# Kernel tuning notes

Hardware: AMD Instinct MI355X
Metric: run time of the kernel (lower is better)

## Reference

```python
import jax, jax.numpy as jnp
import numpy as np

B, R, N, E, D, H = 4, 10, 64, 64, 300, 512  # batch, rounds, nodes, neighbours(=nodes), numberbatch_dim, lstm_hidden
SLOPE = 0.2  # LeakyReLU negative slope from config['slope']


def _xavier_uniform(key, shape, gain=1.414):
    fan_in, fan_out = shape[0], shape[1]
    lim = gain * np.sqrt(6.0 / (fan_in + fan_out))
    return jax.random.uniform(key, shape, jnp.float32, -lim, lim)


def setup_inputs() -> dict:
    key = jax.random.key(0)
    k0, k1, k2, k3, k4 = jax.random.split(key, 5)
    return {
        "adj_list": jax.random.normal(k0, (B, R, N, E, D), jnp.float32),
        "original_nodes": jax.random.normal(k1, (B, R, N, D), jnp.float32),
        "ques_embed": jax.random.normal(k2, (B, R, H), jnp.float32),
        "W": _xavier_uniform(k3, (D + H, H)),
        "a": _xavier_uniform(k4, (2 * H, 1)),
    }


def reference(adj_list, original_nodes, ques_embed, W, a):
    d_in = original_nodes.shape[-1]
    h = W.shape[-1]
    # Split W so that concat([x, q]) @ W == x @ Wn + q @ Wq (avoids the explicit
    # repeat + concat in the original torch code; same math).
    Wn, Wq = W[:d_in], W[d_in:]
    q_proj = jnp.einsum('brq,qh->brh', ques_embed, Wq)              # (B,R,H)
    w_original = jnp.einsum('brnd,dh->brnh', original_nodes, Wn) + q_proj[:, :, None, :]      # (B,R,N,H)
    Wh = jnp.einsum('brned,dh->brneh', adj_list, Wn) + q_proj[:, :, None, None, :]            # (B,R,N,E,H)
    a1, a2 = a[:h, 0], a[h:, 0]
    # e[b,r,n,e] = leakyrelu( (w_original @ a1)[b,r,n] + (Wh @ a2)[b,r,n,e] )
    scores = jnp.einsum('brnh,h->brn', w_original, a1)[..., None] + jnp.einsum('brneh,h->brne', Wh, a2)
    scores = jnp.where(scores > 0, scores, SLOPE * scores)
    # Faithful to original: softmax over dim=1 (the rounds axis). Dropout omitted (eval mode).
    attn = jax.nn.softmax(scores, axis=1)                            # (B,R,N,E)
    # h_prime[b,r,i,h] = sum_j attn[b,r,i,j] * w_original[b,r,j,h]  (requires E == N)
    h_prime = jnp.einsum('brij,brjh->brih', attn, w_original)
    return jax.nn.elu(h_prime)  # concat=True branch
```

## Files before the change

### kernel.cpp

```cpp
#include <hip/hip_runtime.h>
#include <math.h>

namespace {
constexpr int B = 4, R = 10, N = 64, E = 64, D = 300, H = 512;
constexpr int BR = B * R;
constexpr int NE = N * E;
constexpr int S = BR * NE;
constexpr float SLOPE = 0.2f;
constexpr int WO_BLOCKS = BR * 8;
constexpr int S2_BLOCKS = S / 64;

constexpr int OFF_V1  = 0;
constexpr int OFF_V2  = OFF_V1 + 300;
constexpr int OFF_U1  = OFF_V2 + 300;
constexpr int OFF_U2  = OFF_U1 + H;
constexpr int OFF_QP  = OFF_U2 + H;
constexpr int OFF_QA1 = OFF_QP + BR * H;
constexpr int OFF_QA2 = OFF_QA1 + BR;
constexpr int OFF_S1  = OFF_QA2 + BR;
constexpr int OFF_RAW = OFF_S1 + BR * N;
constexpr int OFF_WO  = OFF_RAW + S;
}

__device__ inline float waveReduce(float v) {
#pragma unroll
  for (int o = 32; o > 0; o >>= 1) v += __shfl_xor(v, o, 64);
  return v;
}

__device__ inline float dot4(float4 a, float4 b) {
  return a.x * b.x + a.y * b.y + a.z * b.z + a.w * b.w;
}

__global__ __launch_bounds__(64) void k_vecs(const float* __restrict__ W,
                                             const float* __restrict__ a,
                                             float* __restrict__ ws) {
  int row = blockIdx.x;
  int lane = threadIdx.x;
  const float4* rf  = reinterpret_cast<const float4*>(W + (size_t)row * H);
  const float4* a1f = reinterpret_cast<const float4*>(a);
  const float4* a2f = reinterpret_cast<const float4*>(a + H);
  float4 x0 = rf[lane], x1 = rf[64 + lane];
  float4 p0 = a1f[lane], p1 = a1f[64 + lane];
  float4 q0 = a2f[lane], q1 = a2f[64 + lane];
  float s1 = dot4(x0, p0) + dot4(x1, p1);
  float s2 = dot4(x0, q0) + dot4(x1, q1);
  s1 = waveReduce(s1);
  s2 = waveReduce(s2);
  if (lane == 0) {
    if (row < D) { ws[OFF_V1 + row] = s1; ws[OFF_V2 + row] = s2; }
    else         { ws[OFF_U1 + (row - D)] = s1; ws[OFF_U2 + (row - D)] = s2; }
  }
}

__global__ __launch_bounds__(512) void k_qproj_s1(const float* __restrict__ ques,
                                                  const float* __restrict__ W,
                                                  const float* __restrict__ orig,
                                                  float* __restrict__ ws) {
  int br = blockIdx.x, h = threadIdx.x;
  __shared__ float qs[H];
  __shared__ float red[16];
  __shared__ float qa1s;
  qs[h] = ques[(size_t)br * H + h];
  __syncthreads();
  float ac0 = 0.f, ac1 = 0.f, ac2 = 0.f, ac3 = 0.f;
#pragma unroll 4
  for (int q = 0; q < H; q += 4) {
    ac0 = fmaf(qs[q + 0], W[(size_t)(D + q + 0) * H + h], ac0);
    ac1 = fmaf(qs[q + 1], W[(size_t)(D + q + 1) * H + h], ac1);
    ac2 = fmaf(qs[q + 2], W[(size_t)(D + q + 2) * H + h], ac2);
    ac3 = fmaf(qs[q + 3], W[(size_t)(D + q + 3) * H + h], ac3);
  }
  float acc = (ac0 + ac1) + (ac2 + ac3);
  ws[OFF_QP + br * H + h] = acc;
  float p1 = qs[h] * ws[OFF_U1 + h];
  float p2 = qs[h] * ws[OFF_U2 + h];
  p1 = waveReduce(p1);
  p2 = waveReduce(p2);
  int lane = h & 63, wave = h >> 6;
  if (lane == 0) { red[wave] = p1; red[8 + wave] = p2; }
  __syncthreads();
  if (h == 0) {
    float t1 = 0.f, t2 = 0.f;
#pragma unroll
    for (int i = 0; i < 8; ++i) { t1 += red[i]; t2 += red[8 + i]; }
    ws[OFF_QA1 + br] = t1;
    ws[OFF_QA2 + br] = t2;
    qa1s = t1;
  }
  __syncthreads();
  float qa1 = qa1s;
  const float4* vf = reinterpret_cast<const float4*>(ws + OFF_V1);
  float4 va = vf[lane];
  float4 vb = (lane < 11) ? vf[64 + lane] : make_float4(0.f, 0.f, 0.f, 0.f);
  for (int n2 = wave * 8; n2 < wave * 8 + 8; n2 += 2) {
    const float4* rf0 = reinterpret_cast<const float4*>(orig + ((size_t)br * N + n2) * D);
    const float4* rf1 = reinterpret_cast<const float4*>(orig + ((size_t)br * N + n2 + 1) * D);
    float a0 = dot4(rf0[lane], va);
    float a1 = dot4(rf1[lane], va);
    if (lane < 11) {
      a0 += dot4(rf0[64 + lane], vb);
      a1 += dot4(rf1[64 + lane], vb);
    }
#pragma unroll
    for (int o = 32; o > 0; o >>= 1) {
      a0 += __shfl_xor(a0, o, 64);
      a1 += __shfl_xor(a1, o, 64);
    }
    if (lane == 0) {
      ws[OFF_S1 + br * N + n2]     = a0 + qa1;
      ws[OFF_S1 + br * N + n2 + 1] = a1 + qa1;
    }
  }
}

__global__ __launch_bounds__(256) void k_s2_wo(const float* __restrict__ adj,
                                               const float* __restrict__ orig,
                                               const float* __restrict__ W,
                                               float* __restrict__ ws) {
  __shared__ __align__(16) float smem[64 * 30 + 30 * 64];
  int t = threadIdx.x;
  if (blockIdx.x < WO_BLOCKS) {
    int bi = blockIdx.x;
    int br = bi >> 3, h0 = (bi & 7) * 64;
    float* sA = smem;
    float* sB = smem + 1920;
    const float4* sBf = reinterpret_cast<const float4*>(sB);
    int tn = t >> 4, th = t & 15;
    float acc[4][4] = {};
    for (int k0 = 0; k0 < D; k0 += 30) {
      __syncthreads();
      for (int idx = t; idx < 64 * 30; idx += 256) {
        int n = idx / 30, kk = idx % 30;
        sA[idx] = orig[((size_t)br * N + n) * D + k0 + kk];
      }
      for (int idx = t; idx < 30 * 64; idx += 256) {
        int kk = idx >> 6, hh = idx & 63;
        sB[idx] = W[(size_t)(k0 + kk) * H + h0 + hh];
      }
      __syncthreads();
#pragma unroll 5
      for (int kk = 0; kk < 30; ++kk) {
        float av[4];
#pragma unroll
        for (int i = 0; i < 4; ++i) av[i] = sA[(tn * 4 + i) * 30 + kk];
        float4 bv = sBf[kk * 16 + th];
#pragma unroll
        for (int i = 0; i < 4; ++i) {
          acc[i][0] = fmaf(av[i], bv.x, acc[i][0]);
          acc[i][1] = fmaf(av[i], bv.y, acc[i][1]);
          acc[i][2] = fmaf(av[i], bv.z, acc[i][2]);
          acc[i][3] = fmaf(av[i], bv.w, acc[i][3]);
        }
      }
    }
#pragma unroll
    for (int i = 0; i < 4; ++i) {
      int n = tn * 4 + i;
#pragma unroll
      for (int j = 0; j < 4; ++j) {
        int h = h0 + th * 4 + j;
        ws[OFF_WO + ((size_t)br * N + n) * H + h] = acc[i][j] + ws[OFF_QP + br * H + h];
      }
    }
    return;
  }
  for (int i = t; i < 300; i += 256) smem[i] = ws[OFF_V2 + i];
  __syncthreads();
  const float4* v4 = reinterpret_cast<const float4*>(smem);
  int grp = t & 3;
  int row = (blockIdx.x - WO_BLOCKS) * 64 + (t >> 2);
  const float4* ap = reinterpret_cast<const float4*>(adj) + (size_t)row * 75;
  float ac0 = 0.f, ac1 = 0.f;
#pragma unroll
  for (int j = 0; j < 19; ++j) {
    int idx = grp + 4 * j;
    if (j < 18 || grp < 3) {
      float4 x = ap[idx];
      float4 v = v4[idx];
      if (j & 1) ac1 = fmaf(x.x, v.x, fmaf(x.y, v.y, fmaf(x.z, v.z, fmaf(x.w, v.w, ac1))));
      else       ac0 = fmaf(x.x, v.x, fmaf(x.y, v.y, fmaf(x.z, v.z, fmaf(x.w, v.w, ac0))));
    }
  }
  float acc = ac0 + ac1;
  acc += __shfl_xor(acc, 1, 64);
  acc += __shfl_xor(acc, 2, 64);
  if (grp == 0) ws[OFF_RAW + row] = acc;
}

__global__ __launch_bounds__(256) void k_hprime(const float* __restrict__ ws,
                                                float* __restrict__ out) {
  int br = blockIdx.x;
  int b = br / R, r = br % R;
  int t = threadIdx.x;
  __shared__ __align__(16) float sAtt[64 * 64];
  const float* raw = ws + OFF_RAW;
  for (int ne = t; ne < NE; ne += 256) {
    int n = ne >> 6;
    float v[R];
    float m = -1e30f;
#pragma unroll
    for (int rr = 0; rr < R; ++rr) {
      int brr = b * R + rr;
      float sc = raw[(size_t)brr * NE + ne] + ws[OFF_QA2 + brr] + ws[OFF_S1 + brr * N + n];
      sc = sc > 0.f ? sc : SLOPE * sc;
      v[rr] = sc;
      m = fmaxf(m, sc);
    }
    float s = 0.f;
#pragma unroll
    for (int rr = 0; rr < R; ++rr) { v[rr] = __expf(v[rr] - m); s += v[rr]; }
    sAtt[ne] = v[r] / s;
  }
  __syncthreads();
  int h = blockIdx.y * 64 + (t & 63);
  int ig = t >> 6;
  float acc[16] = {};
  const float* wo = ws + OFF_WO + (size_t)br * N * H;
  const float4* sAttf = reinterpret_cast<const float4*>(sAtt);
#pragma unroll 2
  for (int j4 = 0; j4 < 16; ++j4) {
    float w0 = wo[(size_t)(4 * j4 + 0) * H + h];
    float w1 = wo[(size_t)(4 * j4 + 1) * H + h];
    float w2 = wo[(size_t)(4 * j4 + 2) * H + h];
    float w3 = wo[(size_t)(4 * j4 + 3) * H + h];
#pragma unroll
    for (int ii = 0; ii < 16; ++ii) {
      float4 a4 = sAttf[(ig * 16 + ii) * 16 + j4];
      acc[ii] = fmaf(a4.x, w0, fmaf(a4.y, w1, fmaf(a4.z, w2, fmaf(a4.w, w3, acc[ii]))));
    }
  }
#pragma unroll
  for (int ii = 0; ii < 16; ++ii) {
    int i = ig * 16 + ii;
    float x = acc[ii];
    out[((size_t)br * N + i) * H + h] = x > 0.f ? x : expm1f(x);
  }
}

extern "C" void kernel_launch(void* const* d_in, const int* in_sizes, int n_in,
                              void* d_out, int out_size, void* d_ws, size_t ws_size,
                              hipStream_t stream) {
  const float* adj  = (const float*)d_in[0];
  const float* orig = (const float*)d_in[1];
  const float* ques = (const float*)d_in[2];
  const float* W    = (const float*)d_in[3];
  const float* a    = (const float*)d_in[4];
  float* out = (float*)d_out;
  float* ws  = (float*)d_ws;

  k_vecs<<<dim3(D + H), dim3(64), 0, stream>>>(W, a, ws);
  k_qproj_s1<<<dim3(BR), dim3(512), 0, stream>>>(ques, W, orig, ws);
  k_s2_wo<<<dim3(WO_BLOCKS + S2_BLOCKS), dim3(256), 0, stream>>>(adj, orig, W, ws);
  k_hprime<<<dim3(BR, 8), dim3(256), 0, stream>>>(ws, out);
}
```

Baseline: 122.1 us.

## Split round-axis softmax into its own kernel and widen adj dot-product rows

Moves the leaky-ReLU plus rounds-axis softmax out of k_hprime into a separate k_softmax kernel. It runs once per (b, n, e) and writes normalized attention to workspace, so the 8 h-blocks per br no longer recompute all 10 rounds of softmax redundantly. The adj score kernel now uses 8 lanes per row with all loads issued up front, which raises memory-level parallelism and doubles the block count. The cost is one extra kernel launch and an extra workspace round-trip for the attention matrix.

```diff
diff --git a/kernel.cpp b/kernel.cpp
--- a/kernel.cpp
+++ b/kernel.cpp
@@ -8,7 +8,8 @@
 constexpr int S = BR * NE;
 constexpr float SLOPE = 0.2f;
 constexpr int WO_BLOCKS = BR * 8;
-constexpr int S2_BLOCKS = S / 64;
+constexpr int S2_ROWS = 32;
+constexpr int S2_BLOCKS = S / S2_ROWS;
 
 constexpr int OFF_V1  = 0;
 constexpr int OFF_V2  = OFF_V1 + 300;
@@ -19,7 +20,8 @@
 constexpr int OFF_QA2 = OFF_QA1 + BR;
 constexpr int OFF_S1  = OFF_QA2 + BR;
 constexpr int OFF_RAW = OFF_S1 + BR * N;
-constexpr int OFF_WO  = OFF_RAW + S;
+constexpr int OFF_SC  = OFF_RAW + S;
+constexpr int OFF_WO  = OFF_SC + S;
 }
 
 __device__ inline float waveReduce(float v) {
@@ -114,10 +116,10 @@
   }
 }
 
-__global__ __launch_bounds__(256) void k_s2_wo(const float* __restrict__ adj,
-                                               const float* __restrict__ orig,
-                                               const float* __restrict__ W,
-                                               float* __restrict__ ws) {
+__global__ __launch_bounds__(256) void k_s2wo(const float* __restrict__ adj,
+                                              const float* __restrict__ orig,
+                                              const float* __restrict__ W,
+                                              float* __restrict__ ws) {
   __shared__ __align__(16) float smem[64 * 30 + 30 * 64];
   int t = threadIdx.x;
   if (blockIdx.x < WO_BLOCKS) {
@@ -168,53 +170,61 @@
   for (int i = t; i < 300; i += 256) smem[i] = ws[OFF_V2 + i];
   __syncthreads();
   const float4* v4 = reinterpret_cast<const float4*>(smem);
-  int grp = t & 3;
-  int row = (blockIdx.x - WO_BLOCKS) * 64 + (t >> 2);
+  int row = (blockIdx.x - WO_BLOCKS) * S2_ROWS + (t >> 3);
+  int g = t & 7;
   const float4* ap = reinterpret_cast<const float4*>(adj) + (size_t)row * 75;
-  float ac0 = 0.f, ac1 = 0.f;
-#pragma unroll
-  for (int j = 0; j < 19; ++j) {
-    int idx = grp + 4 * j;
-    if (j < 18 || grp < 3) {
-      float4 x = ap[idx];
-      float4 v = v4[idx];
-      if (j & 1) ac1 = fmaf(x.x, v.x, fmaf(x.y, v.y, fmaf(x.z, v.z, fmaf(x.w, v.w, ac1))));
-      else       ac0 = fmaf(x.x, v.x, fmaf(x.y, v.y, fmaf(x.z, v.z, fmaf(x.w, v.w, ac0))));
-    }
-  }
-  float acc = ac0 + ac1;
+  float4 L0 = ap[g +  0], L1 = ap[g +  8], L2 = ap[g + 16];
+  float4 L3 = ap[g + 24], L4 = ap[g + 32], L5 = ap[g + 40];
+  float4 L6 = ap[g + 48], L7 = ap[g + 56], L8 = ap[g + 64];
+  float4 L9 = make_float4(0.f, 0.f, 0.f, 0.f);
+  float4 V9 = L9;
+  if (g < 3) { L9 = ap[g + 72]; V9 = v4[g + 72]; }
+  float4 V0 = v4[g +  0], V1 = v4[g +  8], V2 = v4[g + 16];
+  float4 V3 = v4[g + 24], V4 = v4[g + 32], V5 = v4[g + 40];
+  float4 V6 = v4[g + 48], V7 = v4[g + 56], V8 = v4[g + 64];
+  float a0 = dot4(L0, V0) + dot4(L2, V2) + dot4(L4, V4) + dot4(L6, V6) + dot4(L8, V8);
+  float a1 = dot4(L1, V1) + dot4(L3, V3) + dot4(L5, V5) + dot4(L7, V7) + dot4(L9, V9);
+  float acc = a0 + a1;
   acc += __shfl_xor(acc, 1, 64);
   acc += __shfl_xor(acc, 2, 64);
-  if (grp == 0) ws[OFF_RAW + row] = acc;
+  acc += __shfl_xor(acc, 4, 64);
+  if (g == 0) ws[OFF_RAW + row] = acc;
+}
+
+__global__ __launch_bounds__(256) void k_softmax(float* __restrict__ ws) {
+  int t = blockIdx.x * 256 + threadIdx.x;
+  int b = t >> 12;
+  int ne = t & 4095;
+  int n = ne >> 6;
+  const float* raw = ws + OFF_RAW;
+  float v[R];
+  float m = -1e30f;
+#pragma unroll
+  for (int r = 0; r < R; ++r) {
+    int br = b * R + r;
+    float sc = raw[(size_t)br * NE + ne] + ws[OFF_QA2 + br] + ws[OFF_S1 + br * N + n];
+    sc = sc > 0.f ? sc : SLOPE * sc;
+    v[r] = sc;
+    m = fmaxf(m, sc);
+  }
+  float s = 0.f;
+#pragma unroll
+  for (int r = 0; r < R; ++r) { v[r] = __expf(v[r] - m); s += v[r]; }
+  float inv = 1.f / s;
+#pragma unroll
+  for (int r = 0; r < R; ++r)
+    ws[OFF_SC + (size_t)(b * R + r) * NE + ne] = v[r] * inv;
 }
 
 __global__ __launch_bounds__(256) void k_hprime(const float* __restrict__ ws,
                                                 float* __restrict__ out) {
   int br = blockIdx.x;
-  int b = br / R, r = br % R;
-  int t = threadIdx.x;
+  int h = blockIdx.y * 64 + (threadIdx.x & 63);
+  int ig = threadIdx.x >> 6;
   __shared__ __align__(16) float sAtt[64 * 64];
-  const float* raw = ws + OFF_RAW;
-  for (int ne = t; ne < NE; ne += 256) {
-    int n = ne >> 6;
-    float v[R];
-    float m = -1e30f;
-#pragma unroll
-    for (int rr = 0; rr < R; ++rr) {
-      int brr = b * R + rr;
-      float sc = raw[(size_t)brr * NE + ne] + ws[OFF_QA2 + brr] + ws[OFF_S1 + brr * N + n];
-      sc = sc > 0.f ? sc : SLOPE * sc;
-      v[rr] = sc;
-      m = fmaxf(m, sc);
-    }
-    float s = 0.f;
-#pragma unroll
-    for (int rr = 0; rr < R; ++rr) { v[rr] = __expf(v[rr] - m); s += v[rr]; }
-    sAtt[ne] = v[r] / s;
-  }
-  __syncthreads();
-  int h = blockIdx.y * 64 + (t & 63);
-  int ig = t >> 6;
+  const float* att = ws + OFF_SC + (size_t)br * NE;
+  for (int idx = threadIdx.x; idx < 4096; idx += 256) sAtt[idx] = att[idx];
+  __syncthreads();
   float acc[16] = {};
   const float* wo = ws + OFF_WO + (size_t)br * N * H;
   const float4* sAttf = reinterpret_cast<const float4*>(sAtt);
@@ -251,6 +261,7 @@
 
   k_vecs<<<dim3(D + H), dim3(64), 0, stream>>>(W, a, ws);
   k_qproj_s1<<<dim3(BR), dim3(512), 0, stream>>>(ques, W, orig, ws);
-  k_s2_wo<<<dim3(WO_BLOCKS + S2_BLOCKS), dim3(256), 0, stream>>>(adj, orig, W, ws);
+  k_s2wo<<<dim3(WO_BLOCKS + S2_BLOCKS), dim3(256), 0, stream>>>(adj, orig, W, ws);
+  k_softmax<<<dim3(B * NE / 256), dim3(256), 0, stream>>>(ws);
   k_hprime<<<dim3(BR, 8), dim3(256), 0, stream>>>(ws, out);
 }
```

After: 115.5 us. 5.4% less time.
